# Kernel optimization log

Hardware: AMD Instinct MI355X
Metric: run time of the kernel (lower is better)

The kernel has to match this reference:

```python
import jax, jax.numpy as jnp
import numpy as np

B, NS, NQ = 128, 128, 512
D_IN, D_OUT = 256, 64


def setup_inputs() -> dict:
    key = jax.random.key(0)
    ks = jax.random.split(key, 6)
    return {
        "phi_support": jax.random.normal(ks[0], (B, NS, D_IN), dtype=jnp.float32),
        "y_support": jax.random.normal(ks[1], (B, NS, D_OUT), dtype=jnp.float32),
        "phi_query": jax.random.normal(ks[2], (B, NQ, D_IN), dtype=jnp.float32),
        "y_query": jax.random.normal(ks[3], (B, NQ, D_OUT), dtype=jnp.float32),
        # xavier-uniform-ish params
        "m_prior": jax.random.uniform(ks[4], (D_IN, D_OUT), minval=-1.0, maxval=1.0) * np.sqrt(6.0 / (D_IN + D_OUT)),
        "S_inv_prior_asym": jax.random.uniform(ks[5], (D_IN, D_IN), minval=-1.0, maxval=1.0) * np.sqrt(6.0 / (2 * D_IN)),
        "sig_eps": jnp.array([0.1], dtype=jnp.float32),
    }


def reference(phi_support, y_support, phi_query, y_query, m_prior, S_inv_prior_asym, sig_eps):
    alpha = 1.0
    d_out = m_prior.shape[1]
    # prior precision (symmetric PSD by construction) and natural-param prior mean
    S_inv_prior = alpha * (S_inv_prior_asym @ S_inv_prior_asym.T)          # [D_in, D_in]
    m_prior_nat = S_inv_prior @ m_prior                                     # [D_in, D_out]
    # posterior precision / covariance per task (nobs > 0 branch)
    S_inv = jnp.einsum('bni,bnj->bij', phi_support, phi_support) + S_inv_prior  # [B, D_in, D_in]
    S = jnp.linalg.inv(S_inv)                                               # batched small inverse
    rhs = jnp.einsum('bni,bnk->bik', phi_support, y_support) + m_prior_nat  # [B, D_in, D_out]
    m = S @ rhs                                                             # [B, D_in, D_out]
    # predictive mean and spread
    mu = phi_query @ m                                                      # [B, Q, D_out]
    spread_fac = 1.0 + jnp.einsum('bqi,bij,bqj->bq', phi_query, S, phi_query)  # [B, Q]
    # sig = spread_fac (x) (eye * sig_eps) : diagonal [B, Q, D_out, D_out]
    diag = jnp.eye(d_out, dtype=mu.dtype) * sig_eps                         # [D_out, D_out]
    sig = spread_fac[..., None, None] * diag
    # nll: logdet of diagonal sig + quadratic form with its inverse (diag -> reciprocal)
    logdet = d_out * (jnp.log(spread_fac) + jnp.log(sig_eps))               # [B, Q]
    resid = y_query - mu
    quadf = jnp.sum(resid * resid, axis=-1) / (spread_fac * sig_eps)        # [B, Q]
    nll = logdet.mean() + quadf.mean()
    return mu, sig, nll
```

## Files before the change

kernel.cpp:

```cpp
#include <hip/hip_runtime.h>
#include <math.h>

#define B_T   128
#define NS    128
#define NQ    512
#define DIN   256
#define DOUT  64

#define MU_SIZE  (B_T*NQ*DOUT)
#define SIG_SIZE (B_T*NQ*DOUT*DOUT)
#define NLL_IDX  (MU_SIZE + SIG_SIZE)

__global__ __launch_bounds__(256) void k_prior_sp(const float* __restrict__ A,
                                                  double* __restrict__ Sp) {
    __shared__ float Ai[16][260];
    __shared__ float Aj[16][260];
    int bi = blockIdx.x;
    int i0 = (bi >> 4) << 4;
    int j0 = (bi & 15) << 4;
    int tid = threadIdx.x;
    for (int idx = tid; idx < 16 * 256; idx += 256) {
        int r = idx >> 8, c = idx & 255;
        Ai[r][c] = A[(i0 + r) * 256 + c];
        Aj[r][c] = A[(j0 + r) * 256 + c];
    }
    __syncthreads();
    int r = tid >> 4, c = tid & 15;
    double acc = 0.0;
    for (int k = 0; k < 256; ++k)
        acc += (double)Ai[r][k] * (double)Aj[c][k];
    Sp[(i0 + r) * 256 + (j0 + c)] = acc;
}

__global__ __launch_bounds__(64) void k_prior_mpn(const double* __restrict__ Sp,
                                                  const float* __restrict__ MP,
                                                  double* __restrict__ MPN) {
    int i = blockIdx.x, k = threadIdx.x;
    double acc = 0.0;
    for (int t = 0; t < 256; ++t)
        acc += Sp[i * 256 + t] * (double)MP[t * 64 + k];
    MPN[i * 64 + k] = acc;
}

__global__ __launch_bounds__(256) void k_build_G(const float* __restrict__ PHI,
                                                 const double* __restrict__ Sp,
                                                 double* __restrict__ G) {
    __shared__ float As[128][64];
    __shared__ float Bs[128][64];
    int b = blockIdx.x;
    int by = blockIdx.y;
    int ti = 0;
    while (((ti + 1) * (ti + 2)) / 2 <= by) ti++;
    int tj = by - (ti * (ti + 1)) / 2;
    int i0 = ti * 64, j0 = tj * 64;
    int tid = threadIdx.x;
    const float* Pb = PHI + b * (NS * DIN);
    for (int idx = tid; idx < 128 * 64; idx += 256) {
        int n = idx >> 6, c = idx & 63;
        As[n][c] = Pb[n * 256 + i0 + c];
        Bs[n][c] = Pb[n * 256 + j0 + c];
    }
    __syncthreads();
    int tx = tid & 15, ty = tid >> 4;
    double acc[4][4];
#pragma unroll
    for (int r = 0; r < 4; ++r)
#pragma unroll
        for (int s = 0; s < 4; ++s) acc[r][s] = 0.0;
    for (int n = 0; n < 128; ++n) {
        float a0 = As[n][4 * ty + 0], a1 = As[n][4 * ty + 1];
        float a2 = As[n][4 * ty + 2], a3 = As[n][4 * ty + 3];
        float b0 = Bs[n][4 * tx + 0], b1 = Bs[n][4 * tx + 1];
        float b2 = Bs[n][4 * tx + 2], b3 = Bs[n][4 * tx + 3];
        acc[0][0] += (double)a0 * b0; acc[0][1] += (double)a0 * b1;
        acc[0][2] += (double)a0 * b2; acc[0][3] += (double)a0 * b3;
        acc[1][0] += (double)a1 * b0; acc[1][1] += (double)a1 * b1;
        acc[1][2] += (double)a1 * b2; acc[1][3] += (double)a1 * b3;
        acc[2][0] += (double)a2 * b0; acc[2][1] += (double)a2 * b1;
        acc[2][2] += (double)a2 * b2; acc[2][3] += (double)a2 * b3;
        acc[3][0] += (double)a3 * b0; acc[3][1] += (double)a3 * b1;
        acc[3][2] += (double)a3 * b2; acc[3][3] += (double)a3 * b3;
    }
    double* Gb = G + b * 65536;
#pragma unroll
    for (int r = 0; r < 4; ++r) {
        int i = i0 + 4 * ty + r;
#pragma unroll
        for (int s = 0; s < 4; ++s) {
            int j = j0 + 4 * tx + s;
            Gb[i * 256 + j] = acc[r][s] + Sp[i * 256 + j];
        }
    }
}

__global__ __launch_bounds__(256) void k_build_rhs(const float* __restrict__ PHI,
                                                   const float* __restrict__ Y,
                                                   const double* __restrict__ MPN,
                                                   double* __restrict__ RHS) {
    __shared__ float As[128][64];
    __shared__ float Ys[128][64];
    int b = blockIdx.x, i0 = blockIdx.y * 64, tid = threadIdx.x;
    const float* Pb = PHI + b * (NS * DIN);
    const float* Yb = Y + b * (NS * DOUT);
    for (int idx = tid; idx < 128 * 64; idx += 256) {
        int n = idx >> 6, c = idx & 63;
        As[n][c] = Pb[n * 256 + i0 + c];
        Ys[n][c] = Yb[n * 64 + c];
    }
    __syncthreads();
    int tx = tid & 15, ty = tid >> 4;
    double acc[4][4];
#pragma unroll
    for (int r = 0; r < 4; ++r)
#pragma unroll
        for (int s = 0; s < 4; ++s) acc[r][s] = 0.0;
    for (int n = 0; n < 128; ++n) {
        float a0 = As[n][4 * ty + 0], a1 = As[n][4 * ty + 1];
        float a2 = As[n][4 * ty + 2], a3 = As[n][4 * ty + 3];
        float y0 = Ys[n][4 * tx + 0], y1 = Ys[n][4 * tx + 1];
        float y2 = Ys[n][4 * tx + 2], y3 = Ys[n][4 * tx + 3];
        acc[0][0] += (double)a0 * y0; acc[0][1] += (double)a0 * y1;
        acc[0][2] += (double)a0 * y2; acc[0][3] += (double)a0 * y3;
        acc[1][0] += (double)a1 * y0; acc[1][1] += (double)a1 * y1;
        acc[1][2] += (double)a1 * y2; acc[1][3] += (double)a1 * y3;
        acc[2][0] += (double)a2 * y0; acc[2][1] += (double)a2 * y1;
        acc[2][2] += (double)a2 * y2; acc[2][3] += (double)a2 * y3;
        acc[3][0] += (double)a3 * y0; acc[3][1] += (double)a3 * y1;
        acc[3][2] += (double)a3 * y2; acc[3][3] += (double)a3 * y3;
    }
    double* Rb = RHS + b * 16384;
#pragma unroll
    for (int r = 0; r < 4; ++r) {
        int i = i0 + 4 * ty + r;
#pragma unroll
        for (int s = 0; s < 4; ++s) {
            int kc = 4 * tx + s;
            Rb[i * 64 + kc] = acc[r][s] + MPN[i * 64 + kc];
        }
    }
}

__global__ __launch_bounds__(256) void k_chol(double* __restrict__ G,
                                              double* __restrict__ LT,
                                              double* __restrict__ INVD) {
    __shared__ double P[8][256];
    int b = blockIdx.x, tid = threadIdx.x;
    double* Gb = G + b * 65536;
    double* LTb = LT + b * 65536;
    for (int k0 = 0; k0 < 256; k0 += 8) {
#pragma unroll
        for (int p = 0; p < 8; ++p) P[p][tid] = Gb[tid * 256 + k0 + p];
        __syncthreads();
        for (int p = 0; p < 8; ++p) {
            int k = k0 + p;
            if (tid >= k) {
                double v = P[p][tid];
                for (int p2 = 0; p2 < p; ++p2) v -= P[p2][tid] * P[p2][k];
                P[p][tid] = v;
            }
            __syncthreads();
            double d = sqrt(fmax(P[p][k], 1e-300));
            double inv = 1.0 / d;
            if (tid > k) P[p][tid] *= inv;
            else if (tid == k) { P[p][tid] = d; INVD[b * 256 + k] = inv; }
            __syncthreads();
        }
#pragma unroll
        for (int p = 0; p < 8; ++p) {
            int k = k0 + p;
            if (tid >= k) LTb[k * 256 + tid] = P[p][tid];
        }
        int ty = tid >> 4, tx = tid & 15;
        for (int i = k0 + 8 + ty; i < 256; i += 16) {
            double pi[8];
#pragma unroll
            for (int p = 0; p < 8; ++p) pi[p] = P[p][i];
            for (int j = k0 + 8 + tx; j <= i; j += 16) {
                double g = Gb[i * 256 + j];
#pragma unroll
                for (int p = 0; p < 8; ++p) g -= pi[p] * P[p][j];
                Gb[i * 256 + j] = g;
            }
        }
        __syncthreads();
    }
}

__global__ __launch_bounds__(256) void k_trinv(const double* __restrict__ LT,
                                               double* __restrict__ TI,
                                               float* __restrict__ TIF) {
    __shared__ double SHD[8192];
    int b = blockIdx.x, tid = threadIdx.x;
    const double* LTb = LT + b * 65536;
    double* TIb = TI + b * 65536;
    float* TIFb = TIF + b * 65536;
    for (int idx = tid; idx < 65536; idx += 256) {
        int i = idx >> 8, k = idx & 255;
        if (k > i) { TIb[idx] = 0.0; TIFb[idx] = 0.0f; }
    }
    for (int idx = tid; idx < 8192; idx += 256) {
        int g = idx >> 10, rem = idx & 1023, k = rem >> 5, i = rem & 31;
        SHD[idx] = LTb[(32 * g + k) * 256 + 32 * g + i];
    }
    __syncthreads();
    {
        int g = tid >> 5, j = tid & 31;
        const double* D = SHD + g * 1024;
        double x[32];
#pragma unroll
        for (int i = 0; i < 32; ++i) {
            double s = (i == j) ? 1.0 : 0.0;
#pragma unroll
            for (int k = 0; k < i; ++k) {
                double lv = D[k * 32 + i];
                s -= (k >= j) ? lv * x[k] : 0.0;
            }
            double inv = 1.0 / D[i * 32 + i];
            x[i] = (i >= j) ? s * inv : 0.0;
        }
#pragma unroll
        for (int i = 0; i < 32; ++i) {
            int gi = 32 * g + i, gj = 32 * g + j;
            TIb[gi * 256 + gj] = x[i];
            TIFb[gi * 256 + gj] = (float)x[i];
        }
    }
    __syncthreads();
    double* Bsh = SHD;
    int j = tid & 31, ig = tid >> 5;
    for (int I = 1; I < 8; ++I) {
        for (int J = I - 1; J >= 0; --J) {
            double acc[4] = {0.0, 0.0, 0.0, 0.0};
            for (int K = J; K < I; ++K) {
                for (int kk = 0; kk < 32; ++kk) {
                    double tv = TIb[(32 * K + kk) * 256 + 32 * J + j];
#pragma unroll
                    for (int r = 0; r < 4; ++r) {
                        double lv = LTb[(32 * K + kk) * 256 + 32 * I + ig * 4 + r];
                        acc[r] += lv * tv;
                    }
                }
            }
            __syncthreads();
#pragma unroll
            for (int r = 0; r < 4; ++r) Bsh[(ig * 4 + r) * 32 + j] = acc[r];
            __syncthreads();
            double c[4] = {0.0, 0.0, 0.0, 0.0};
            for (int k = 0; k < 32; ++k) {
                double bv = Bsh[k * 32 + j];
#pragma unroll
                for (int r = 0; r < 4; ++r) {
                    double dv = TIb[(32 * I + ig * 4 + r) * 256 + 32 * I + k];
                    c[r] -= dv * bv;
                }
            }
#pragma unroll
            for (int r = 0; r < 4; ++r) {
                int gi = 32 * I + ig * 4 + r, gj = 32 * J + j;
                TIb[gi * 256 + gj] = c[r];
                TIFb[gi * 256 + gj] = (float)c[r];
            }
        }
        __syncthreads();
    }
}

__global__ __launch_bounds__(256) void k_gemm_Z(const double* __restrict__ TI,
                                                const double* __restrict__ RHS,
                                                double* __restrict__ Z) {
    __shared__ double As[32][64];
    __shared__ double Bs[64][64];
    int b = blockIdx.x, i0 = blockIdx.y * 32;
    int tid = threadIdx.x, c = tid & 63, rg = tid >> 6;
    const double* TIb = TI + b * 65536;
    const double* Rb = RHS + b * 16384;
    double* Zb = Z + b * 16384;
    double acc[8] = {};
    for (int k0 = 0; k0 <= i0; k0 += 64) {
        for (int idx = tid; idx < 2048; idx += 256) {
            int r = idx >> 6, kk = idx & 63;
            As[r][kk] = TIb[(i0 + r) * 256 + k0 + kk];
        }
        for (int idx = tid; idx < 4096; idx += 256) {
            int kk = idx >> 6, cc = idx & 63;
            Bs[kk][cc] = Rb[(k0 + kk) * 64 + cc];
        }
        __syncthreads();
        for (int kk = 0; kk < 64; ++kk) {
            double bv = Bs[kk][c];
#pragma unroll
            for (int r = 0; r < 8; ++r)
                acc[r] += As[rg * 8 + r][kk] * bv;
        }
        __syncthreads();
    }
#pragma unroll
    for (int r = 0; r < 8; ++r)
        Zb[(i0 + rg * 8 + r) * 64 + c] = acc[r];
}

__global__ __launch_bounds__(256) void k_gemm_M(const double* __restrict__ TI,
                                                const double* __restrict__ Z,
                                                double* __restrict__ M) {
    __shared__ double As[64][32];
    __shared__ double Bs[64][64];
    int b = blockIdx.x, i0 = blockIdx.y * 32;
    int tid = threadIdx.x, c = tid & 63, rg = tid >> 6;
    const double* TIb = TI + b * 65536;
    const double* Zb = Z + b * 16384;
    double* Mb = M + b * 16384;
    double acc[8] = {};
    for (int k0 = (i0 >> 6) << 6; k0 < 256; k0 += 64) {
        for (int idx = tid; idx < 2048; idx += 256) {
            int kk = idx >> 5, ri = idx & 31;
            As[kk][ri] = TIb[(k0 + kk) * 256 + i0 + ri];
        }
        for (int idx = tid; idx < 4096; idx += 256) {
            int kk = idx >> 6, cc = idx & 63;
            Bs[kk][cc] = Zb[(k0 + kk) * 64 + cc];
        }
        __syncthreads();
        for (int kk = 0; kk < 64; ++kk) {
            double bv = Bs[kk][c];
#pragma unroll
            for (int r = 0; r < 8; ++r)
                acc[r] += As[kk][rg * 8 + r] * bv;
        }
        __syncthreads();
    }
#pragma unroll
    for (int r = 0; r < 8; ++r)
        Mb[(i0 + rg * 8 + r) * 64 + c] = acc[r];
}

__global__ __launch_bounds__(256) void k_spread_gemm(const float* __restrict__ PHIQ,
                                                     const float* __restrict__ TIF,
                                                     float* __restrict__ PSUM) {
    __shared__ float Qs[64][65];
    __shared__ float Ts[64][65];
    int b = blockIdx.x, q0 = blockIdx.y * 64, I = blockIdx.z, i0 = I * 64;
    int tid = threadIdx.x, tx = tid & 15, ty = tid >> 4;
    const float* Qb = PHIQ + b * (NQ * DIN) + q0 * DIN;
    const float* Tb = TIF + b * 65536;
    float acc[4][4];
#pragma unroll
    for (int r = 0; r < 4; ++r)
#pragma unroll
        for (int s = 0; s < 4; ++s) acc[r][s] = 0.0f;
    for (int k0 = 0; k0 <= i0; k0 += 64) {
        for (int idx = tid; idx < 4096; idx += 256) {
            int r = idx >> 6, c = idx & 63;
            Qs[r][c] = Qb[r * 256 + k0 + c];
            Ts[c][r] = Tb[(i0 + r) * 256 + k0 + c];
        }
        __syncthreads();
        for (int kk = 0; kk < 64; ++kk) {
            float a0 = Qs[4 * ty + 0][kk], a1 = Qs[4 * ty + 1][kk];
            float a2 = Qs[4 * ty + 2][kk], a3 = Qs[4 * ty + 3][kk];
            float b0 = Ts[kk][4 * tx + 0], b1 = Ts[kk][4 * tx + 1];
            float b2 = Ts[kk][4 * tx + 2], b3 = Ts[kk][4 * tx + 3];
            acc[0][0] += a0 * b0; acc[0][1] += a0 * b1; acc[0][2] += a0 * b2; acc[0][3] += a0 * b3;
            acc[1][0] += a1 * b0; acc[1][1] += a1 * b1; acc[1][2] += a1 * b2; acc[1][3] += a1 * b3;
            acc[2][0] += a2 * b0; acc[2][1] += a2 * b1; acc[2][2] += a2 * b2; acc[2][3] += a2 * b3;
            acc[3][0] += a3 * b0; acc[3][1] += a3 * b1; acc[3][2] += a3 * b2; acc[3][3] += a3 * b3;
        }
        __syncthreads();
    }
#pragma unroll
    for (int r = 0; r < 4; ++r) {
        float p = acc[r][0] * acc[r][0] + acc[r][1] * acc[r][1]
                + acc[r][2] * acc[r][2] + acc[r][3] * acc[r][3];
        p += __shfl_down(p, 8, 16);
        p += __shfl_down(p, 4, 16);
        p += __shfl_down(p, 2, 16);
        p += __shfl_down(p, 1, 16);
        if (tx == 0) PSUM[(size_t)(b * 4 + I) * 512 + q0 + 4 * ty + r] = p;
    }
}

__global__ __launch_bounds__(256) void k_spread_combine(const float* __restrict__ PSUM,
                                                        float* __restrict__ SPREAD) {
    int b = blockIdx.x;
    for (int q = threadIdx.x; q < 512; q += 256) {
        float s = 1.0f;
#pragma unroll
        for (int I = 0; I < 4; ++I) s += PSUM[(size_t)(b * 4 + I) * 512 + q];
        SPREAD[b * 512 + q] = s;
    }
}

__global__ __launch_bounds__(256) void k_mu(const float* __restrict__ PHIQ,
                                            const double* __restrict__ M,
                                            float* __restrict__ MU) {
    __shared__ float Qs[64][65];
    __shared__ float Ms[64][64];
    int b = blockIdx.x, q0 = blockIdx.y * 64, tid = threadIdx.x;
    int tx = tid & 15, ty = tid >> 4;
    const float* Qb = PHIQ + b * (NQ * DIN) + q0 * DIN;
    const double* Mb = M + b * 16384;
    float acc[4][4];
#pragma unroll
    for (int r = 0; r < 4; ++r)
#pragma unroll
        for (int s = 0; s < 4; ++s) acc[r][s] = 0.0f;
    for (int c0 = 0; c0 < 256; c0 += 64) {
        for (int idx = tid; idx < 4096; idx += 256) {
            int r = idx >> 6, c = idx & 63;
            Qs[r][c] = Qb[r * 256 + c0 + c];
            Ms[r][c] = (float)Mb[(c0 + r) * 64 + c];
        }
        __syncthreads();
        for (int kk = 0; kk < 64; ++kk) {
            float a0 = Qs[4 * ty + 0][kk], a1 = Qs[4 * ty + 1][kk];
            float a2 = Qs[4 * ty + 2][kk], a3 = Qs[4 * ty + 3][kk];
            float b0 = Ms[kk][4 * tx + 0], b1 = Ms[kk][4 * tx + 1];
            float b2 = Ms[kk][4 * tx + 2], b3 = Ms[kk][4 * tx + 3];
            acc[0][0] += a0 * b0; acc[0][1] += a0 * b1; acc[0][2] += a0 * b2; acc[0][3] += a0 * b3;
            acc[1][0] += a1 * b0; acc[1][1] += a1 * b1; acc[1][2] += a1 * b2; acc[1][3] += a1 * b3;
            acc[2][0] += a2 * b0; acc[2][1] += a2 * b1; acc[2][2] += a2 * b2; acc[2][3] += a2 * b3;
            acc[3][0] += a3 * b0; acc[3][1] += a3 * b1; acc[3][2] += a3 * b2; acc[3][3] += a3 * b3;
        }
        __syncthreads();
    }
#pragma unroll
    for (int r = 0; r < 4; ++r) {
        float4 v = make_float4(acc[r][0], acc[r][1], acc[r][2], acc[r][3]);
        *(float4*)&MU[(b * NQ + q0 + 4 * ty + r) * 64 + 4 * tx] = v;
    }
}

__global__ __launch_bounds__(256) void k_nll_part(const float* __restrict__ YQ,
                                                  const float* __restrict__ MU,
                                                  const float* __restrict__ SPREAD,
                                                  const float* __restrict__ SE,
                                                  double* __restrict__ NLLP) {
    __shared__ double red[256];
    int tid = threadIdx.x;
    int bq = blockIdx.x * 256 + tid;
    float se = SE[0];
    float sp = SPREAD[bq];
    float qs = 0.0f;
    const float4* y4 = (const float4*)(YQ + bq * 64);
    const float4* m4 = (const float4*)(MU + bq * 64);
#pragma unroll
    for (int t = 0; t < 16; ++t) {
        float4 y = y4[t], m = m4[t];
        float dx = y.x - m.x, dy = y.y - m.y, dz = y.z - m.z, dw = y.w - m.w;
        qs += dx * dx + dy * dy + dz * dz + dw * dw;
    }
    float val = 64.0f * (logf(sp) + logf(se)) + qs / (sp * se);
    red[tid] = (double)val;
    __syncthreads();
    for (int s = 128; s > 0; s >>= 1) {
        if (tid < s) red[tid] += red[tid + s];
        __syncthreads();
    }
    if (tid == 0) NLLP[blockIdx.x] = red[0] * (1.0 / 65536.0);
}

__global__ __launch_bounds__(256) void k_nll_final(const double* __restrict__ NLLP,
                                                   float* __restrict__ out) {
    __shared__ double red[256];
    int tid = threadIdx.x;
    red[tid] = NLLP[tid];
    __syncthreads();
    for (int s = 128; s > 0; s >>= 1) {
        if (tid < s) red[tid] += red[tid + s];
        __syncthreads();
    }
    if (tid == 0) out[NLL_IDX] = (float)red[0];
}

__global__ __launch_bounds__(256) void k_sig(const float* __restrict__ SPREAD,
                                             const float* __restrict__ SE,
                                             float* __restrict__ out) {
    __shared__ float sv_s;
    int bq = blockIdx.x, tid = threadIdx.x;
    if (tid == 0) sv_s = SPREAD[bq] * SE[0];
    __syncthreads();
    float sv = sv_s;
    float* base = out + (size_t)MU_SIZE + (size_t)bq * 4096;
    int i = tid >> 2;
    int jb = (tid & 3) << 4;
    int d = i - jb;
    float vals[16];
#pragma unroll
    for (int t = 0; t < 16; ++t) vals[t] = (t == d) ? sv : 0.0f;
    float4* p = (float4*)(base + tid * 16);
    p[0] = make_float4(vals[0], vals[1], vals[2], vals[3]);
    p[1] = make_float4(vals[4], vals[5], vals[6], vals[7]);
    p[2] = make_float4(vals[8], vals[9], vals[10], vals[11]);
    p[3] = make_float4(vals[12], vals[13], vals[14], vals[15]);
}

extern "C" void kernel_launch(void* const* d_in, const int* in_sizes, int n_in,
                              void* d_out, int out_size, void* d_ws, size_t ws_size,
                              hipStream_t stream) {
    const float* PHI_S = (const float*)d_in[0];
    const float* Y_S   = (const float*)d_in[1];
    const float* PHI_Q = (const float*)d_in[2];
    const float* Y_Q   = (const float*)d_in[3];
    const float* MP    = (const float*)d_in[4];
    const float* AP    = (const float*)d_in[5];
    const float* SE    = (const float*)d_in[6];
    float* out = (float*)d_out;

    double* scratch = (double*)(out + MU_SIZE);
    double* G    = scratch;
    double* LT   = G + 8388608;
    double* RHS  = LT + 8388608;
    double* Z    = RHS + 2097152;
    double* TI   = Z + 2097152;
    double* Spd  = TI + 8388608;
    double* MPN  = Spd + 65536;
    double* INVD = MPN + 16384;
    float*  TIF  = (float*)(INVD + 32768);
    float*  PSUM = TIF + 8388608;
    float*  SPREAD = (float*)d_ws;
    double* NLLP   = (double*)((char*)d_ws + 65536 * 4);

    k_prior_sp      <<<256, 256, 0, stream>>>(AP, Spd);
    k_prior_mpn     <<<256, 64, 0, stream>>>(Spd, MP, MPN);
    k_build_G       <<<dim3(B_T, 10), 256, 0, stream>>>(PHI_S, Spd, G);
    k_build_rhs     <<<dim3(B_T, 4), 256, 0, stream>>>(PHI_S, Y_S, MPN, RHS);
    k_chol          <<<B_T, 256, 0, stream>>>(G, LT, INVD);
    k_trinv         <<<B_T, 256, 0, stream>>>(LT, TI, TIF);
    k_gemm_Z        <<<dim3(B_T, 8), 256, 0, stream>>>(TI, RHS, Z);
    k_gemm_M        <<<dim3(B_T, 8), 256, 0, stream>>>(TI, Z, RHS);
    k_spread_gemm   <<<dim3(B_T, 8, 4), 256, 0, stream>>>(PHI_Q, TIF, PSUM);
    k_spread_combine<<<B_T, 256, 0, stream>>>(PSUM, SPREAD);
    k_mu            <<<dim3(B_T, 8), 256, 0, stream>>>(PHI_Q, RHS, out);
    k_nll_part      <<<256, 256, 0, stream>>>(Y_Q, out, SPREAD, SE, NLLP);
    k_nll_final     <<<1, 256, 0, stream>>>(NLLP, out);
    k_sig           <<<65536, 256, 0, stream>>>(SPREAD, SE, out);
}
```

Before: 2.502 ms.

## Fuse Cholesky with triangular inverse, widen panel, fuse mu with NLL

Merges the Cholesky and triangular-inverse kernels into one per-batch kernel. The Cholesky panel width grows from 8 to 16, with a 2x2 register-blocked trailing update. The spread-combine and NLL partial kernels fold into the mu GEMM epilogue, which uses an atomic double accumulator zeroed in the first kernel. This removes several launches and the MU/SPREAD round trips through global memory, at the cost of larger shared-memory use and a nondeterministic atomic reduction order.

Result: faster. 2.244 ms (-10.3%).

```diff
diff --git a/kernel.cpp b/kernel.cpp
--- a/kernel.cpp
+++ b/kernel.cpp
@@ -12,13 +12,15 @@
 #define NLL_IDX  (MU_SIZE + SIG_SIZE)
 
 __global__ __launch_bounds__(256) void k_prior_sp(const float* __restrict__ A,
-                                                  double* __restrict__ Sp) {
+                                                  double* __restrict__ Sp,
+                                                  double* __restrict__ NLLACC) {
     __shared__ float Ai[16][260];
     __shared__ float Aj[16][260];
     int bi = blockIdx.x;
     int i0 = (bi >> 4) << 4;
     int j0 = (bi & 15) << 4;
     int tid = threadIdx.x;
+    if (bi == 0 && tid == 0) NLLACC[0] = 0.0;
     for (int idx = tid; idx < 16 * 256; idx += 256) {
         int r = idx >> 8, c = idx & 255;
         Ai[r][c] = A[(i0 + r) * 256 + c];
@@ -140,60 +142,68 @@
     }
 }
 
-__global__ __launch_bounds__(256) void k_chol(double* __restrict__ G,
-                                              double* __restrict__ LT,
-                                              double* __restrict__ INVD) {
-    __shared__ double P[8][256];
+__global__ __launch_bounds__(256) void k_cholinv(double* __restrict__ G,
+                                                 double* __restrict__ LT,
+                                                 double* __restrict__ TI,
+                                                 float* __restrict__ TIF) {
+    __shared__ double S[8192];
     int b = blockIdx.x, tid = threadIdx.x;
     double* Gb = G + b * 65536;
     double* LTb = LT + b * 65536;
-    for (int k0 = 0; k0 < 256; k0 += 8) {
-#pragma unroll
-        for (int p = 0; p < 8; ++p) P[p][tid] = Gb[tid * 256 + k0 + p];
-        __syncthreads();
-        for (int p = 0; p < 8; ++p) {
+    double* TIb = TI + b * 65536;
+    float* TIFb = TIF + b * 65536;
+
+    double* P = S;
+#define PCH(p, r) P[(p) * 258 + (r)]
+    for (int k0 = 0; k0 < 256; k0 += 16) {
+        int rows = 256 - k0;
+        for (int idx = tid; idx < rows * 16; idx += 256) {
+            int r = k0 + (idx >> 4), p = idx & 15;
+            PCH(p, r) = Gb[r * 256 + k0 + p];
+        }
+        __syncthreads();
+        for (int p = 0; p < 16; ++p) {
             int k = k0 + p;
             if (tid >= k) {
-                double v = P[p][tid];
-                for (int p2 = 0; p2 < p; ++p2) v -= P[p2][tid] * P[p2][k];
-                P[p][tid] = v;
+                double v = PCH(p, tid);
+                for (int p2 = 0; p2 < p; ++p2) v -= PCH(p2, tid) * PCH(p2, k);
+                PCH(p, tid) = v;
             }
             __syncthreads();
-            double d = sqrt(fmax(P[p][k], 1e-300));
+            double d = sqrt(fmax(PCH(p, k), 1e-300));
             double inv = 1.0 / d;
-            if (tid > k) P[p][tid] *= inv;
-            else if (tid == k) { P[p][tid] = d; INVD[b * 256 + k] = inv; }
+            if (tid > k) PCH(p, tid) *= inv;
+            else if (tid == k) PCH(p, tid) = d;
             __syncthreads();
         }
-#pragma unroll
-        for (int p = 0; p < 8; ++p) {
+        for (int p = 0; p < 16; ++p) {
             int k = k0 + p;
-            if (tid >= k) LTb[k * 256 + tid] = P[p][tid];
+            if (tid >= k) LTb[k * 256 + tid] = PCH(p, tid);
         }
         int ty = tid >> 4, tx = tid & 15;
-        for (int i = k0 + 8 + ty; i < 256; i += 16) {
-            double pi[8];
-#pragma unroll
-            for (int p = 0; p < 8; ++p) pi[p] = P[p][i];
-            for (int j = k0 + 8 + tx; j <= i; j += 16) {
-                double g = Gb[i * 256 + j];
-#pragma unroll
-                for (int p = 0; p < 8; ++p) g -= pi[p] * P[p][j];
-                Gb[i * 256 + j] = g;
+        for (int i2 = k0 + 16 + 2 * ty; i2 < 256; i2 += 32) {
+            double pa[16], pb[16];
+#pragma unroll
+            for (int p = 0; p < 16; ++p) { pa[p] = PCH(p, i2); pb[p] = PCH(p, i2 + 1); }
+            for (int j2 = k0 + 16 + 2 * tx; j2 <= i2 + 1; j2 += 32) {
+                double g00 = 0.0, g01 = 0.0, g10 = 0.0, g11 = 0.0;
+#pragma unroll
+                for (int p = 0; p < 16; ++p) {
+                    double q0 = PCH(p, j2), q1 = PCH(p, j2 + 1);
+                    g00 += pa[p] * q0; g01 += pa[p] * q1;
+                    g10 += pb[p] * q0; g11 += pb[p] * q1;
+                }
+                if (j2 <= i2)     Gb[i2 * 256 + j2]           -= g00;
+                if (j2 + 1 <= i2) Gb[i2 * 256 + j2 + 1]       -= g01;
+                Gb[(i2 + 1) * 256 + j2] -= g10;
+                if (j2 <= i2)     Gb[(i2 + 1) * 256 + j2 + 1] -= g11;
             }
         }
         __syncthreads();
     }
-}
-
-__global__ __launch_bounds__(256) void k_trinv(const double* __restrict__ LT,
-                                               double* __restrict__ TI,
-                                               float* __restrict__ TIF) {
-    __shared__ double SHD[8192];
-    int b = blockIdx.x, tid = threadIdx.x;
-    const double* LTb = LT + b * 65536;
-    double* TIb = TI + b * 65536;
-    float* TIFb = TIF + b * 65536;
+#undef PCH
+
+    double* SHD = S;
     for (int idx = tid; idx < 65536; idx += 256) {
         int i = idx >> 8, k = idx & 255;
         if (k > i) { TIb[idx] = 0.0; TIFb[idx] = 0.0f; }
@@ -378,22 +388,17 @@
     }
 }
 
-__global__ __launch_bounds__(256) void k_spread_combine(const float* __restrict__ PSUM,
-                                                        float* __restrict__ SPREAD) {
-    int b = blockIdx.x;
-    for (int q = threadIdx.x; q < 512; q += 256) {
-        float s = 1.0f;
-#pragma unroll
-        for (int I = 0; I < 4; ++I) s += PSUM[(size_t)(b * 4 + I) * 512 + q];
-        SPREAD[b * 512 + q] = s;
-    }
-}
-
-__global__ __launch_bounds__(256) void k_mu(const float* __restrict__ PHIQ,
-                                            const double* __restrict__ M,
-                                            float* __restrict__ MU) {
+__global__ __launch_bounds__(256) void k_mu_nll(const float* __restrict__ PHIQ,
+                                                const double* __restrict__ M,
+                                                const float* __restrict__ YQ,
+                                                const float* __restrict__ PSUM,
+                                                const float* __restrict__ SE,
+                                                float* __restrict__ SPREAD,
+                                                double* __restrict__ NLLACC,
+                                                float* __restrict__ MU) {
     __shared__ float Qs[64][65];
     __shared__ float Ms[64][64];
+    __shared__ double nred[64];
     int b = blockIdx.x, q0 = blockIdx.y * 64, tid = threadIdx.x;
     int tx = tid & 15, ty = tid >> 4;
     const float* Qb = PHIQ + b * (NQ * DIN) + q0 * DIN;
@@ -422,53 +427,40 @@
         }
         __syncthreads();
     }
+    float se = SE[0];
 #pragma unroll
     for (int r = 0; r < 4; ++r) {
+        int q = q0 + 4 * ty + r;
         float4 v = make_float4(acc[r][0], acc[r][1], acc[r][2], acc[r][3]);
-        *(float4*)&MU[(b * NQ + q0 + 4 * ty + r) * 64 + 4 * tx] = v;
-    }
-}
-
-__global__ __launch_bounds__(256) void k_nll_part(const float* __restrict__ YQ,
-                                                  const float* __restrict__ MU,
-                                                  const float* __restrict__ SPREAD,
-                                                  const float* __restrict__ SE,
-                                                  double* __restrict__ NLLP) {
-    __shared__ double red[256];
-    int tid = threadIdx.x;
-    int bq = blockIdx.x * 256 + tid;
-    float se = SE[0];
-    float sp = SPREAD[bq];
-    float qs = 0.0f;
-    const float4* y4 = (const float4*)(YQ + bq * 64);
-    const float4* m4 = (const float4*)(MU + bq * 64);
-#pragma unroll
-    for (int t = 0; t < 16; ++t) {
-        float4 y = y4[t], m = m4[t];
-        float dx = y.x - m.x, dy = y.y - m.y, dz = y.z - m.z, dw = y.w - m.w;
-        qs += dx * dx + dy * dy + dz * dz + dw * dw;
-    }
-    float val = 64.0f * (logf(sp) + logf(se)) + qs / (sp * se);
-    red[tid] = (double)val;
-    __syncthreads();
-    for (int s = 128; s > 0; s >>= 1) {
-        if (tid < s) red[tid] += red[tid + s];
-        __syncthreads();
-    }
-    if (tid == 0) NLLP[blockIdx.x] = red[0] * (1.0 / 65536.0);
-}
-
-__global__ __launch_bounds__(256) void k_nll_final(const double* __restrict__ NLLP,
-                                                   float* __restrict__ out) {
-    __shared__ double red[256];
-    int tid = threadIdx.x;
-    red[tid] = NLLP[tid];
-    __syncthreads();
-    for (int s = 128; s > 0; s >>= 1) {
-        if (tid < s) red[tid] += red[tid + s];
-        __syncthreads();
-    }
-    if (tid == 0) out[NLL_IDX] = (float)red[0];
+        *(float4*)&MU[(b * NQ + q) * 64 + 4 * tx] = v;
+        float4 y = *(const float4*)&YQ[(size_t)(b * NQ + q) * 64 + 4 * tx];
+        float dx = y.x - v.x, dy = y.y - v.y, dz = y.z - v.z, dw = y.w - v.w;
+        float qs = dx * dx + dy * dy + dz * dz + dw * dw;
+        qs += __shfl_down(qs, 8, 16);
+        qs += __shfl_down(qs, 4, 16);
+        qs += __shfl_down(qs, 2, 16);
+        qs += __shfl_down(qs, 1, 16);
+        if (tx == 0) {
+            float sp = 1.0f + PSUM[(size_t)(b * 4 + 0) * 512 + q]
+                            + PSUM[(size_t)(b * 4 + 1) * 512 + q]
+                            + PSUM[(size_t)(b * 4 + 2) * 512 + q]
+                            + PSUM[(size_t)(b * 4 + 3) * 512 + q];
+            SPREAD[b * 512 + q] = sp;
+            float val = 64.0f * (logf(sp) + logf(se)) + qs / (sp * se);
+            nred[ty * 4 + r] = (double)val;
+        }
+    }
+    __syncthreads();
+    for (int s = 32; s > 0; s >>= 1) {
+        if (tid < s) nred[tid] += nred[tid + s];
+        __syncthreads();
+    }
+    if (tid == 0) atomicAdd(NLLACC, nred[0] * (1.0 / 65536.0));
+}
+
+__global__ void k_nll_final(const double* __restrict__ NLLACC,
+                            float* __restrict__ out) {
+    if (threadIdx.x == 0) out[NLL_IDX] = (float)NLLACC[0];
 }
 
 __global__ __launch_bounds__(256) void k_sig(const float* __restrict__ SPREAD,
@@ -513,24 +505,21 @@
     double* TI   = Z + 2097152;
     double* Spd  = TI + 8388608;
     double* MPN  = Spd + 65536;
-    double* INVD = MPN + 16384;
-    float*  TIF  = (float*)(INVD + 32768);
+    float*  TIF  = (float*)(MPN + 16384);
     float*  PSUM = TIF + 8388608;
     float*  SPREAD = (float*)d_ws;
-    double* NLLP   = (double*)((char*)d_ws + 65536 * 4);
-
-    k_prior_sp      <<<256, 256, 0, stream>>>(AP, Spd);
-    k_prior_mpn     <<<256, 64, 0, stream>>>(Spd, MP, MPN);
-    k_build_G       <<<dim3(B_T, 10), 256, 0, stream>>>(PHI_S, Spd, G);
-    k_build_rhs     <<<dim3(B_T, 4), 256, 0, stream>>>(PHI_S, Y_S, MPN, RHS);
-    k_chol          <<<B_T, 256, 0, stream>>>(G, LT, INVD);
-    k_trinv         <<<B_T, 256, 0, stream>>>(LT, TI, TIF);
-    k_gemm_Z        <<<dim3(B_T, 8), 256, 0, stream>>>(TI, RHS, Z);
-    k_gemm_M        <<<dim3(B_T, 8), 256, 0, stream>>>(TI, Z, RHS);
-    k_spread_gemm   <<<dim3(B_T, 8, 4), 256, 0, stream>>>(PHI_Q, TIF, PSUM);
-    k_spread_combine<<<B_T, 256, 0, stream>>>(PSUM, SPREAD);
-    k_mu            <<<dim3(B_T, 8), 256, 0, stream>>>(PHI_Q, RHS, out);
-    k_nll_part      <<<256, 256, 0, stream>>>(Y_Q, out, SPREAD, SE, NLLP);
-    k_nll_final     <<<1, 256, 0, stream>>>(NLLP, out);
-    k_sig           <<<65536, 256, 0, stream>>>(SPREAD, SE, out);
-}
+    double* NLLACC = (double*)((char*)d_ws + 65536 * 4);
+
+    k_prior_sp   <<<256, 256, 0, stream>>>(AP, Spd, NLLACC);
+    k_prior_mpn  <<<256, 64, 0, stream>>>(Spd, MP, MPN);
+    k_build_G    <<<dim3(B_T, 10), 256, 0, stream>>>(PHI_S, Spd, G);
+    k_build_rhs  <<<dim3(B_T, 4), 256, 0, stream>>>(PHI_S, Y_S, MPN, RHS);
+    k_cholinv    <<<B_T, 256, 0, stream>>>(G, LT, TI, TIF);
+    k_gemm_Z     <<<dim3(B_T, 8), 256, 0, stream>>>(TI, RHS, Z);
+    k_gemm_M     <<<dim3(B_T, 8), 256, 0, stream>>>(TI, Z, RHS);
+    k_spread_gemm<<<dim3(B_T, 8, 4), 256, 0, stream>>>(PHI_Q, TIF, PSUM);
+    k_mu_nll     <<<dim3(B_T, 8), 256, 0, stream>>>(PHI_Q, RHS, Y_Q, PSUM, SE,
+                                                    SPREAD, NLLACC, out);
+    k_nll_final  <<<1, 64, 0, stream>>>(NLLACC, out);
+    k_sig        <<<65536, 256, 0, stream>>>(SPREAD, SE, out);
+}
```
